# Kernel optimization log

Hardware: AMD Instinct MI355X
Metric: run time of the kernel (lower is better)

## Reference

```python
import jax, jax.numpy as jnp
import numpy as np

NEG_INIT = -1.0e9


def setup_inputs() -> dict:
    key = jax.random.key(0)
    k1, k2, k3, k4, k5, k6, k7 = jax.random.split(key, 7)
    N, D, d_att, G = 262144, 512, 128, 512
    feats = jax.random.normal(k1, (N, D), dtype=jnp.float32)
    index = jnp.sort(jax.random.randint(k2, (N,), 0, G, dtype=jnp.int64))
    # torch Linear params: weight (out,in), bias (out,)
    Vw = jax.random.normal(k3, (d_att, D), dtype=jnp.float32) / np.sqrt(D)
    Vb = jax.random.normal(k4, (d_att,), dtype=jnp.float32) * 0.01
    Uw = jax.random.normal(k5, (d_att, D), dtype=jnp.float32) / np.sqrt(D)
    Ub = jax.random.normal(k6, (d_att,), dtype=jnp.float32) * 0.01
    ww = jax.random.normal(k7, (1, d_att), dtype=jnp.float32) / np.sqrt(d_att)
    return {"feats": feats, "index": index, "num_groups": G,
            "Vw": Vw, "Vb": Vb, "Uw": Uw, "Ub": Ub, "ww": ww}


def reference(feats, index, num_groups, Vw, Vb, Uw, Ub, ww):
    # gated attention MLP: A = tanh(V x) * sigmoid(U x); scores = w A
    A = jnp.tanh(feats @ Vw.T + Vb) * jax.nn.sigmoid(feats @ Uw.T + Ub)  # (N, d_att)
    scores = (A @ ww.T)[:, 0]  # (N,)
    # segment max with -1e9 init (matches scatter_reduce amax include_self)
    max_per_group = jax.ops.segment_max(scores, index, num_segments=num_groups)
    max_per_group = jnp.maximum(max_per_group, NEG_INIT)  # empty segments -> -1e9
    exp_scores = jnp.exp(scores - max_per_group[index])
    denom = jax.ops.segment_sum(exp_scores, index, num_segments=num_groups)
    weights = exp_scores / (denom[index] + 1e-8)
    # weighted scatter-sum pooling: (num_groups, D)
    out = jax.ops.segment_sum(feats * weights[:, None], index, num_segments=num_groups)
    return out
```

## Files before the change

### kernel.cpp

```cpp
#include <hip/hip_runtime.h>
#include <hip/hip_fp8.h>
#include <cstddef>

#define NEG_INIT -1.0e9f

typedef _Float16 f16x8 __attribute__((ext_vector_type(8)));
typedef _Float16 f16x4 __attribute__((ext_vector_type(4)));
typedef _Float16 f16x2 __attribute__((ext_vector_type(2)));
typedef float f32x4 __attribute__((ext_vector_type(4)));

constexpr int D   = 512;
constexpr int BM  = 32;
constexpr int BK  = 32;
constexpr int NKS = D / BK;
constexpr int SSK = 4;
constexpr int NSS = NKS / SSK;
constexpr int LDH  = 520;
constexpr int LDRB = 520;
constexpr int PS  = 516;
constexpr float RSC  = 2048.f;
constexpr float RISC = 1.f / 2048.f;

#define BAR_LGKM()                                            \
    do {                                                      \
        asm volatile("s_waitcnt lgkmcnt(0)" ::: "memory");    \
        __builtin_amdgcn_s_barrier();                         \
        asm volatile("" ::: "memory");                        \
    } while (0)

#if __has_builtin(__builtin_amdgcn_cvt_pk_fp8_f32) && __has_builtin(__builtin_amdgcn_cvt_f32_fp8)
#define HW_FP8 1
#else
#define HW_FP8 0
#endif

__device__ __forceinline__ unsigned int pack_fp8x4(float r0, float r1,
                                                   float r2, float r3) {
#if HW_FP8
    int p = __builtin_amdgcn_cvt_pk_fp8_f32(r0, r1, 0, false);
    p     = __builtin_amdgcn_cvt_pk_fp8_f32(r2, r3, p, true);
    return (unsigned int)p;
#else
    __hip_fp8_e4m3 q0(r0), q1(r1), q2(r2), q3(r3);
    return (unsigned int)q0.__x | ((unsigned int)q1.__x << 8) |
           ((unsigned int)q2.__x << 16) | ((unsigned int)q3.__x << 24);
#endif
}

template <int SEL>
__device__ __forceinline__ float unpack_fp8(unsigned int word) {
#if HW_FP8
    return __builtin_amdgcn_cvt_f32_fp8((int)word, SEL);
#else
    __hip_fp8_e4m3 q;
    q.__x = (unsigned char)(word >> (8 * SEL));
    return (float)q;
#endif
}

__device__ __forceinline__ float fast_tanh(float v) {
    float e2 = __expf(2.f * v);
    return 1.f - 2.f * __builtin_amdgcn_rcpf(e2 + 1.f);
}
__device__ __forceinline__ float fast_sigmoid(float u) {
    return __builtin_amdgcn_rcpf(1.f + __expf(-u));
}

__global__ __launch_bounds__(64) void k_wprep(const float* __restrict__ Vw,
                                              const float* __restrict__ Uw,
                                              _Float16* __restrict__ Wfrag) {
    const int bid  = blockIdx.x;
    const int lane = threadIdx.x;
    const int j    = bid & 3;
    const int ks   = (bid >> 2) & 15;
    const int wc   = bid >> 6;
    const int l15  = lane & 15;
    const int kgrp = lane >> 4;
    const float* src = (j < 2 ? Vw + (size_t)(wc * 32 + j * 16 + l15) * D
                              : Uw + (size_t)(wc * 32 + (j - 2) * 16 + l15) * D)
                       + ks * BK + kgrp * 8;
    f16x8 h;
    #pragma unroll
    for (int e = 0; e < 8; ++e) h[e] = (_Float16)src[e];
    *(f16x8*)(Wfrag + ((size_t)bid * 64 + lane) * 8) = h;
}

__global__ __launch_bounds__(256) void k_bounds(const int* __restrict__ index,
                                                int N, int G,
                                                int* __restrict__ start) {
    int g = blockIdx.x * blockDim.x + threadIdx.x;
    if (g > G) return;
    int lo = 0, hi = N;
    while (lo < hi) {
        int mid = (lo + hi) >> 1;
        if (index[mid] < g) lo = mid + 1; else hi = mid;
    }
    start[g] = lo;
}

__global__ __launch_bounds__(512, 6) void k_fused(
    const float* __restrict__ feats, const _Float16* __restrict__ Wfrag,
    const float* __restrict__ Vb, const float* __restrict__ Ub,
    const float* __restrict__ ww, const int* __restrict__ index,
    const int* __restrict__ start, float* __restrict__ P, int N)
{
    __shared__ __align__(16) _Float16 Xh[BM][LDH];
    __shared__ __align__(8)  unsigned char Xr8[BM * LDRB];
    __shared__ float sred[8][BM];
    __shared__ float srow[BM];
    __shared__ float evals[BM];

    const int t    = threadIdx.x;
    const int lane = t & 63;
    const int wc   = t >> 6;
    const int l15  = lane & 15;
    const int kgrp = lane >> 4;
    const int blk  = blockIdx.x;
    const int rb   = blk * BM;

    const int srw  = t >> 4;
    const int scol = (t & 15) * 8;
    const float* xg = feats + (size_t)(rb + srw) * D + scol;

    float4 xa[2][2];
    auto issueX = [&](int ss) {
        const float* p = xg + ss * 128;
        xa[ss & 1][0] = *(const float4*)p;
        xa[ss & 1][1] = *(const float4*)(p + 4);
    };
    auto commitX = [&](int ss) {
        const int c0 = ss * 128 + scol;
        float v[8];
        v[0] = xa[ss & 1][0].x; v[1] = xa[ss & 1][0].y;
        v[2] = xa[ss & 1][0].z; v[3] = xa[ss & 1][0].w;
        v[4] = xa[ss & 1][1].x; v[5] = xa[ss & 1][1].y;
        v[6] = xa[ss & 1][1].z; v[7] = xa[ss & 1][1].w;
        f16x8 h;
        float res[8];
        #pragma unroll
        for (int e = 0; e < 8; ++e) {
            h[e] = (_Float16)v[e];
            res[e] = (v[e] - (float)h[e]) * RSC;
        }
        unsigned int rp0 = pack_fp8x4(res[0], res[1], res[2], res[3]);
        unsigned int rp1 = pack_fp8x4(res[4], res[5], res[6], res[7]);
        *(f16x8*)&Xh[srw][c0] = h;
        uint2 rw = {rp0, rp1};
        *(uint2*)&Xr8[srw * LDRB + c0] = rw;
    };

    const _Float16* wbV = Wfrag + (size_t)(wc >> 1) * 32768
                                + (size_t)(wc & 1) * 512 + (size_t)lane * 8;
    const _Float16* wbU = wbV + 1024;

    f32x4 accV[2], accU[2];
    #pragma unroll
    for (int i = 0; i < 2; ++i) {
        accV[i] = (f32x4){0.f, 0.f, 0.f, 0.f};
        accU[i] = (f32x4){0.f, 0.f, 0.f, 0.f};
    }

    issueX(0); issueX(1);
    commitX(0);
    BAR_LGKM();

    #pragma unroll
    for (int ss = 0; ss < NSS; ++ss) {
        if (ss + 2 < NSS) issueX(ss + 2);
        #pragma unroll
        for (int k2 = 0; k2 < SSK; ++k2) {
            const int ks = ss * SSK + k2;
            f16x8 bv = *(const f16x8*)(wbV + (size_t)ks * 2048);
            f16x8 bu = *(const f16x8*)(wbU + (size_t)ks * 2048);
            f16x8 ha[2];
            #pragma unroll
            for (int i = 0; i < 2; ++i)
                ha[i] = *(const f16x8*)&Xh[i * 16 + l15][ks * BK + kgrp * 8];
            #pragma unroll
            for (int i = 0; i < 2; ++i) {
                accV[i] = __builtin_amdgcn_mfma_f32_16x16x32_f16(ha[i], bv, accV[i], 0, 0, 0);
                accU[i] = __builtin_amdgcn_mfma_f32_16x16x32_f16(ha[i], bu, accU[i], 0, 0, 0);
            }
        }
        if (ss + 1 < NSS) {
            commitX(ss + 1);
            BAR_LGKM();
        }
    }

    {
        const int c = wc * 16 + l15;
        const float vb = Vb[c], ub = Ub[c], w = ww[c];
        float part[2][4];
        #pragma unroll
        for (int i = 0; i < 2; ++i)
            #pragma unroll
            for (int r = 0; r < 4; ++r) {
                float v = accV[i][r] + vb;
                float u = accU[i][r] + ub;
                part[i][r] = w * fast_tanh(v) * fast_sigmoid(u);
            }
        #pragma unroll
        for (int off = 1; off < 16; off <<= 1)
            #pragma unroll
            for (int i = 0; i < 2; ++i)
                #pragma unroll
                for (int r = 0; r < 4; ++r)
                    part[i][r] += __shfl_xor(part[i][r], off);
        if (l15 == 0) {
            #pragma unroll
            for (int i = 0; i < 2; ++i)
                #pragma unroll
                for (int r = 0; r < 4; ++r)
                    sred[wc][i * 16 + kgrp * 4 + r] = part[i][r];
        }
    }
    __syncthreads();
    if (t < BM) {
        float s = sred[0][t];
        #pragma unroll
        for (int w8 = 1; w8 < 8; ++w8) s += sred[w8][t];
        srow[t] = s;
    }
    __syncthreads();

    const int gl = index[rb];
    const int gh = index[rb + BM - 1];
    for (int g = gl + wc; g <= gh; g += 8) {
        const int r0 = max(start[g], rb), r1 = min(start[g + 1], rb + BM);
        if (r1 <= r0) continue;
        const bool in = (lane >= r0 - rb) && (lane < r1 - rb);
        float m = in ? srow[lane] : NEG_INIT;
        #pragma unroll
        for (int off = 32; off; off >>= 1) m = fmaxf(m, __shfl_xor(m, off));
        float e = in ? expf(srow[lane] - m) : 0.f;
        if (in) evals[lane] = e;
        float s = e;
        #pragma unroll
        for (int off = 32; off; off >>= 1) s += __shfl_xor(s, off);
        if (lane == 0) {
            float* slot = P + (size_t)(blk + g) * PS;
            slot[0] = m; slot[1] = s;
        }
    }
    __syncthreads();

    if (t < 256) {
        const int c0 = t * 2;
        for (int g = gl; g <= gh; ++g) {
            const int r0 = max(start[g], rb), r1 = min(start[g + 1], rb + BM);
            if (r1 <= r0) continue;
            float a0 = 0.f, a1 = 0.f;
            for (int r = r0; r < r1; ++r) {
                const int rr = r - rb;
                const float e = evals[rr];
                f16x2 hp = *(const f16x2*)&Xh[rr][c0];
                unsigned int rv = *(const unsigned short*)&Xr8[rr * LDRB + c0];
                float x0 = fmaf(unpack_fp8<0>(rv), RISC, (float)hp[0]);
                float x1 = fmaf(unpack_fp8<1>(rv), RISC, (float)hp[1]);
                a0 = fmaf(e, x0, a0);
                a1 = fmaf(e, x1, a1);
            }
            float2 o = {a0, a1};
            *(float2*)(P + (size_t)(blk + g) * PS + 4 + c0) = o;
        }
    }
}

__global__ __launch_bounds__(512) void k_merge(const float* __restrict__ P,
                                               const int* __restrict__ start,
                                               float* __restrict__ out)
{
    const int g = blockIdx.x, t = threadIdx.x;
    const int s0 = start[g], s1 = start[g + 1];
    if (s0 >= s1) { out[(size_t)g * D + t] = 0.f; return; }
    const int b0 = s0 >> 5, b1 = (s1 - 1) >> 5;
    float M = NEG_INIT;
    for (int b = b0; b <= b1; ++b)
        M = fmaxf(M, P[(size_t)(b + g) * PS]);
    float den = 0.f, acc = 0.f;
    for (int b = b0; b <= b1; ++b) {
        const float* slot = P + (size_t)(b + g) * PS;
        float w = expf(slot[0] - M);
        den += w * slot[1];
        acc += w * slot[4 + t];
    }
    out[(size_t)g * D + t] = acc / (den + 1e-8f);
}

extern "C" void kernel_launch(void* const* d_in, const int* in_sizes, int n_in,
                              void* d_out, int out_size, void* d_ws, size_t ws_size,
                              hipStream_t stream) {
    const float* feats = (const float*)d_in[0];
    const int*   index = (const int*)d_in[1];
    const float* Vw = (const float*)d_in[3];
    const float* Vb = (const float*)d_in[4];
    const float* Uw = (const float*)d_in[5];
    const float* Ub = (const float*)d_in[6];
    const float* ww = (const float*)d_in[7];
    float* out = (float*)d_out;

    const int N = in_sizes[1];
    const int G = out_size / D;
    const int nblk = (N + BM - 1) / BM;

    _Float16* Wfrag = (_Float16*)d_ws;
    int* start      = (int*)(Wfrag + (size_t)256 * 512);
    size_t off      = (size_t)256 * 512 * 2 + (G + 1) * 4;
    off             = (off + 15) & ~(size_t)15;
    float* P        = (float*)((char*)d_ws + off);

    hipLaunchKernelGGL(k_wprep, dim3(256), dim3(64), 0, stream, Vw, Uw, Wfrag);
    hipLaunchKernelGGL(k_bounds, dim3((G + 1 + 255) / 256), dim3(256), 0, stream,
                       index, N, G, start);
    hipLaunchKernelGGL(k_fused, dim3(nblk), dim3(512), 0, stream,
                       feats, Wfrag, Vb, Ub, ww, index, start, P, N);
    hipLaunchKernelGGL(k_merge, dim3(G), dim3(512), 0, stream, P, start, out);
}
```

Measured before the change: 206.6 us.

## Deepen X prefetch to three stages, use fast exp, spread pooling over all threads

Feature prefetch now keeps three stages of register buffers in flight instead of two, so more global load latency can hide behind the MFMA loop at the cost of extra registers. The accurate expf calls in the softmax and merge kernels become the __expf intrinsic, trading some precision for cheaper math. The weighted pooling stage now has all 512 threads handle one column each instead of 256 threads handling two, which spreads the work but uses narrower LDS accesses.

```diff
diff --git a/kernel.cpp b/kernel.cpp
--- a/kernel.cpp
+++ b/kernel.cpp
@@ -6,7 +6,6 @@
 
 typedef _Float16 f16x8 __attribute__((ext_vector_type(8)));
 typedef _Float16 f16x4 __attribute__((ext_vector_type(4)));
-typedef _Float16 f16x2 __attribute__((ext_vector_type(2)));
 typedef float f32x4 __attribute__((ext_vector_type(4)));
 
 constexpr int D   = 512;
@@ -122,19 +121,21 @@
     const int scol = (t & 15) * 8;
     const float* xg = feats + (size_t)(rb + srw) * D + scol;
 
-    float4 xa[2][2];
+    float4 xa[3][2];
     auto issueX = [&](int ss) {
         const float* p = xg + ss * 128;
-        xa[ss & 1][0] = *(const float4*)p;
-        xa[ss & 1][1] = *(const float4*)(p + 4);
+        const int sl = ss % 3;
+        xa[sl][0] = *(const float4*)p;
+        xa[sl][1] = *(const float4*)(p + 4);
     };
     auto commitX = [&](int ss) {
         const int c0 = ss * 128 + scol;
+        const int sl = ss % 3;
         float v[8];
-        v[0] = xa[ss & 1][0].x; v[1] = xa[ss & 1][0].y;
-        v[2] = xa[ss & 1][0].z; v[3] = xa[ss & 1][0].w;
-        v[4] = xa[ss & 1][1].x; v[5] = xa[ss & 1][1].y;
-        v[6] = xa[ss & 1][1].z; v[7] = xa[ss & 1][1].w;
+        v[0] = xa[sl][0].x; v[1] = xa[sl][0].y;
+        v[2] = xa[sl][0].z; v[3] = xa[sl][0].w;
+        v[4] = xa[sl][1].x; v[5] = xa[sl][1].y;
+        v[6] = xa[sl][1].z; v[7] = xa[sl][1].w;
         f16x8 h;
         float res[8];
         #pragma unroll
@@ -160,13 +161,13 @@
         accU[i] = (f32x4){0.f, 0.f, 0.f, 0.f};
     }
 
-    issueX(0); issueX(1);
+    issueX(0); issueX(1); issueX(2);
     commitX(0);
     BAR_LGKM();
 
     #pragma unroll
     for (int ss = 0; ss < NSS; ++ss) {
-        if (ss + 2 < NSS) issueX(ss + 2);
+        if (ss + 3 < NSS) issueX(ss + 3);
         #pragma unroll
         for (int k2 = 0; k2 < SSK; ++k2) {
             const int ks = ss * SSK + k2;
@@ -233,7 +234,7 @@
         float m = in ? srow[lane] : NEG_INIT;
         #pragma unroll
         for (int off = 32; off; off >>= 1) m = fmaxf(m, __shfl_xor(m, off));
-        float e = in ? expf(srow[lane] - m) : 0.f;
+        float e = in ? __expf(srow[lane] - m) : 0.f;
         if (in) evals[lane] = e;
         float s = e;
         #pragma unroll
@@ -245,24 +246,19 @@
     }
     __syncthreads();
 
-    if (t < 256) {
-        const int c0 = t * 2;
+    {
         for (int g = gl; g <= gh; ++g) {
             const int r0 = max(start[g], rb), r1 = min(start[g + 1], rb + BM);
             if (r1 <= r0) continue;
-            float a0 = 0.f, a1 = 0.f;
+            float a = 0.f;
             for (int r = r0; r < r1; ++r) {
                 const int rr = r - rb;
-                const float e = evals[rr];
-                f16x2 hp = *(const f16x2*)&Xh[rr][c0];
-                unsigned int rv = *(const unsigned short*)&Xr8[rr * LDRB + c0];
-                float x0 = fmaf(unpack_fp8<0>(rv), RISC, (float)hp[0]);
-                float x1 = fmaf(unpack_fp8<1>(rv), RISC, (float)hp[1]);
-                a0 = fmaf(e, x0, a0);
-                a1 = fmaf(e, x1, a1);
+                float h = (float)Xh[rr][t];
+                unsigned int rv = Xr8[rr * LDRB + t];
+                float x = fmaf(unpack_fp8<0>(rv), RISC, h);
+                a = fmaf(evals[rr], x, a);
             }
-            float2 o = {a0, a1};
-            *(float2*)(P + (size_t)(blk + g) * PS + 4 + c0) = o;
+            P[(size_t)(blk + g) * PS + 4 + t] = a;
         }
     }
 }
@@ -281,7 +277,7 @@
     float den = 0.f, acc = 0.f;
     for (int b = b0; b <= b1; ++b) {
         const float* slot = P + (size_t)(b + g) * PS;
-        float w = expf(slot[0] - M);
+        float w = __expf(slot[0] - M);
         den += w * slot[1];
         acc += w * slot[4 + t];
     }
```

New measurement: 209.8 us. No clear change (+1.6%).
